# Kernel optimization log

Hardware: AMD Instinct MI355X
Metric: run time of the kernel (lower is better)

Reference implementation:

```python
import jax, jax.numpy as jnp
import numpy as np
import math

B, S, D, H = 2, 2048, 1024, 16
HD = D // H  # head_dim = 64
ROPE_BASE = 100000
EPS = 1e-09


def _linear_init(key, in_f, out_f):
    std = min(1.0, math.sqrt(out_f / in_f)) / math.sqrt(in_f)
    return jax.random.normal(key, (in_f, out_f)) * std


def setup_inputs() -> dict:
    key = jax.random.key(0)
    ks = jax.random.split(key, 7)
    Q = jax.random.normal(ks[0], (B, S, D), dtype=jnp.float32)
    K = jax.random.normal(ks[1], (B, S, D), dtype=jnp.float32)
    V = jax.random.normal(ks[2], (B, S, D), dtype=jnp.float32)
    mask = jnp.tril(jnp.ones((S, S), dtype=bool))  # causal
    Wq = _linear_init(ks[3], D, D)
    Wk = _linear_init(ks[4], D, D)
    Wv = _linear_init(ks[5], D, D)
    Wo = _linear_init(ks[6], D, D)
    return {"Q": Q, "K": K, "V": V, "mask": mask,
            "Wq": Wq, "Wk": Wk, "Wv": Wv, "Wo": Wo}


def _rope_tables(seq_len, d):
    positions = jnp.arange(0, seq_len)
    freqs = ROPE_BASE ** (jnp.arange(0, d, 2) / d)
    gamma = positions[:, None] * (1.0 / freqs)[None, :]  # [t, d/2]
    return jnp.cos(gamma).astype(jnp.bfloat16), jnp.sin(gamma).astype(jnp.bfloat16)


def _apply_rope(x, cos, sin):
    # x: [..., t, d]; cos/sin: [t, d/2]
    d = x.shape[-1]
    x1, x2 = x[..., : d // 2], x[..., d // 2:]
    y1 = x1 * cos + x2 * sin
    y2 = -x1 * sin + x2 * cos
    return jnp.concatenate([y1, y2], axis=-1)


def _rms_norm(x):
    rms = jnp.sqrt(jnp.mean(jnp.square(x), axis=-1, keepdims=True) + EPS)
    return x / rms


def reference(Q, K, V, mask, Wq, Wk, Wv, Wo):
    cos, sin = _rope_tables(S, HD)
    q = jnp.dot(Q, Wq)
    k = jnp.dot(K, Wk)
    v = jnp.dot(V, Wv)
    # [B, S, D] -> [B, H, S, HD]
    split = lambda t: t.reshape(*t.shape[:-1], H, HD).swapaxes(-3, -2)
    q, k, v = split(q), split(k), split(v)
    q = _rms_norm(_apply_rope(q, cos, sin))
    k = _rms_norm(_apply_rope(k, cos, sin))
    logits = jnp.einsum('bhqd,bhkd->bhqk', q, k) / jnp.sqrt(jnp.float32(HD))
    logits = jnp.where(mask[None, None, :, :], logits, -1000000000.0)
    attn = jax.nn.softmax(logits, axis=-1)
    vals = jnp.einsum('bhqk,bhkd->bhqd', attn, v)
    # [B, H, S, HD] -> [B, S, D]
    vals = vals.swapaxes(-3, -2).reshape(B, S, D)
    return jnp.dot(vals, Wo)
```

## Files before the change

### kernel.cpp

```cpp
#include <hip/hip_runtime.h>
#include <hip/hip_bf16.h>
#include <stdint.h>

typedef __hip_bfloat16 bf16;
typedef __attribute__((ext_vector_type(8))) short short8;
typedef __attribute__((ext_vector_type(4))) short short4v;
typedef __attribute__((ext_vector_type(4))) float float4v;

static constexpr int nB = 2, nS = 2048, nD = 1024, nH = 16, nHD = 64;
static constexpr int nBS = nB * nS;

#define AS_GLOBAL __attribute__((address_space(1)))
#define AS_LDS    __attribute__((address_space(3)))

union Frag16B { short8 v; uint4 u4; uint2 u2[2]; };

__device__ __forceinline__ void gload_lds16(const void* g, void* l) {
  __builtin_amdgcn_global_load_lds((AS_GLOBAL uint32_t*)(g), (AS_LDS uint32_t*)(l), 16, 0, 0);
}

__device__ __forceinline__ float fast_exp2(float x) {
#if __has_builtin(__builtin_amdgcn_exp2f)
  return __builtin_amdgcn_exp2f(x);
#else
  float r; asm volatile("v_exp_f32 %0, %1" : "=v"(r) : "v"(x)); return r;
#endif
}

__device__ __forceinline__ void lds_barrier() {
  asm volatile("s_waitcnt lgkmcnt(0)\ns_barrier" ::: "memory");
}

__device__ __forceinline__ void lgkm_wait() {
  asm volatile("s_waitcnt lgkmcnt(0)" ::: "memory");
}

__global__ __launch_bounds__(256) void prep_kernel(
    const float* __restrict__ Qin, const float* __restrict__ Kin, const float* __restrict__ Vin,
    const float* __restrict__ Wq, const float* __restrict__ Wk,
    const float* __restrict__ Wv, const float* __restrict__ Wo,
    bf16* __restrict__ Qbf, bf16* __restrict__ Kbf, bf16* __restrict__ Vbf,
    bf16* __restrict__ WqT, bf16* __restrict__ WkT, bf16* __restrict__ WvT, bf16* __restrict__ WoT,
    bf16* __restrict__ cos_t, bf16* __restrict__ sin_t) {
  __shared__ float tile[64][65];
  int bx = blockIdx.x, t = threadIdx.x;
  if (bx < 3072) {
    int tz = bx >> 10, blk = bx & 1023;
    const float* src = tz == 0 ? Qin : tz == 1 ? Kin : Vin;
    bf16* dst = tz == 0 ? Qbf : tz == 1 ? Kbf : Vbf;
#pragma unroll
    for (int i = 0; i < 4; ++i) {
      int idx = blk * 1024 + i * 256 + t;
      float4 v = ((const float4*)src)[idx];
      union { bf16 b[4]; uint2 u; } tmp;
      tmp.b[0] = __float2bfloat16(v.x);
      tmp.b[1] = __float2bfloat16(v.y);
      tmp.b[2] = __float2bfloat16(v.z);
      tmp.b[3] = __float2bfloat16(v.w);
      ((uint2*)dst)[idx] = tmp.u;
    }
  } else if (bx < 4096) {
    int idx = bx - 3072;
    int z = idx >> 8;
    const float* W = z == 0 ? Wq : z == 1 ? Wk : z == 2 ? Wv : Wo;
    bf16* T = z == 0 ? WqT : z == 1 ? WkT : z == 2 ? WvT : WoT;
    int tk = (idx & 15) * 64, tn = ((idx >> 4) & 15) * 64;
    int c = t & 63, r0 = t >> 6;
#pragma unroll
    for (int i = 0; i < 16; ++i) {
      int r = i * 4 + r0;
      tile[r][c] = W[(size_t)(tk + r) * nD + tn + c];
    }
    __syncthreads();
#pragma unroll
    for (int i = 0; i < 16; ++i) {
      int r = i * 4 + r0;
      T[(size_t)(tn + r) * nD + tk + c] = __float2bfloat16(tile[c][r]);
    }
  } else {
    int base = (bx - 4096) * 1024 + t * 4;
#pragma unroll
    for (int i = 0; i < 4; ++i) {
      int e = base + i;
      int s = e >> 5, j = e & 31;
      float inv_freq = powf(100000.0f, -(float)(2 * j) / 64.0f);
      float g = (float)s * inv_freq;
      cos_t[e] = __float2bfloat16(cosf(g));
      sin_t[e] = __float2bfloat16(sinf(g));
    }
  }
}

__global__ __launch_bounds__(512, 2) void gemm_qkv_kernel(
    const bf16* __restrict__ A0, const bf16* __restrict__ A1, const bf16* __restrict__ A2,
    const bf16* __restrict__ Bt0, const bf16* __restrict__ Bt1, const bf16* __restrict__ Bt2,
    bf16* __restrict__ q_h, bf16* __restrict__ k_h, bf16* __restrict__ vt_h,
    const bf16* __restrict__ cos_t, const bf16* __restrict__ sin_t) {
  const int z = blockIdx.z;
  const bf16* __restrict__ A  = z == 0 ? A0 : (z == 1 ? A1 : A2);
  const bf16* __restrict__ Bt = z == 0 ? Bt0 : (z == 1 ? Bt1 : Bt2);

  __shared__ bf16 As[2 * 256 * 32];
  __shared__ bf16 Bs[2 * 256 * 32];

  const int t = threadIdx.x;
  const int lane = t & 63;
  const int wid = t >> 6;
  const int quad = lane >> 4;
  const int l16 = lane & 15;
  const int wm = wid >> 2;
  const int wn = wid & 3;
  const int m0 = blockIdx.x * 256;
  const int n0 = blockIdx.y * 256;

  const int sc    = (t & 7) ^ ((t >> 3) & 7);
  const int sml   = 2 * (t >> 3) + (sc >> 2);
  const int skoff = (sc & 3) * 8;
  const int swave = wid * 512;

  const int R0a = wm * 64 + (l16 >> 1);
  const int R0b = wn * 32 + (l16 >> 1);
  const int cpar = (l16 & 1) * 4;
  const int abase = R0a * 64 + (((cpar + quad) ^ (R0a & 7)) * 8);
  const int bbase = R0b * 64 + (((cpar + quad) ^ (R0b & 7)) * 8);

#define STAGE_A(KT, BUF) do { \
    const bf16* ag_ = A + (size_t)(m0 + sml) * nD + (KT) * 32 + skoff; \
    gload_lds16(ag_, As + (BUF) + swave); \
    gload_lds16(ag_ + (size_t)128 * nD, As + (BUF) + 4096 + swave); \
  } while (0)
#define STAGE_B(KT, BUF) do { \
    const bf16* bg_ = Bt + (size_t)(n0 + sml) * nD + (KT) * 32 + skoff; \
    gload_lds16(bg_, Bs + (BUF) + swave); \
    gload_lds16(bg_ + (size_t)128 * nD, Bs + (BUF) + 4096 + swave); \
  } while (0)

  float4v acc[8][4] = {};

  STAGE_A(0, 0);
  STAGE_B(0, 0);
  STAGE_A(1, 8192);
  asm volatile("s_waitcnt vmcnt(2)" ::: "memory");
  __builtin_amdgcn_s_barrier();

#pragma unroll 2
  for (int T = 0; T < 32; ++T) {
    const int cu = (T & 1) * 8192;
    const int nx = cu ^ 8192;

    if (T < 31) STAGE_B(T + 1, nx);
    Frag16B fa[4], fb[4];
#pragma unroll
    for (int mi = 0; mi < 4; ++mi) fa[mi].u4 = *(const uint4*)&As[cu + abase + mi * 512];
#pragma unroll
    for (int ni = 0; ni < 4; ++ni) fb[ni].u4 = *(const uint4*)&Bs[cu + bbase + ni * 512];
    __builtin_amdgcn_s_setprio(1);
#pragma unroll
    for (int mi = 0; mi < 4; ++mi)
#pragma unroll
      for (int ni = 0; ni < 4; ++ni)
        acc[mi][ni] = __builtin_amdgcn_mfma_f32_16x16x32_bf16(fa[mi].v, fb[ni].v, acc[mi][ni], 0, 0, 0);
    __builtin_amdgcn_s_setprio(0);
    __builtin_amdgcn_s_barrier();

    Frag16B fa2[4];
#pragma unroll
    for (int mi = 0; mi < 4; ++mi) fa2[mi].u4 = *(const uint4*)&As[cu + abase + (mi + 4) * 512];
    asm volatile("s_waitcnt lgkmcnt(0)" ::: "memory");
    __builtin_amdgcn_s_setprio(1);
#pragma unroll
    for (int mi = 0; mi < 2; ++mi)
#pragma unroll
      for (int ni = 0; ni < 4; ++ni)
        acc[4 + mi][ni] = __builtin_amdgcn_mfma_f32_16x16x32_bf16(fa2[mi].v, fb[ni].v, acc[4 + mi][ni], 0, 0, 0);
    __builtin_amdgcn_s_setprio(0);
    __builtin_amdgcn_s_barrier();

    if (T < 30) STAGE_A(T + 2, cu);
    __builtin_amdgcn_s_setprio(1);
#pragma unroll
    for (int mi = 2; mi < 4; ++mi)
#pragma unroll
      for (int ni = 0; ni < 4; ++ni)
        acc[4 + mi][ni] = __builtin_amdgcn_mfma_f32_16x16x32_bf16(fa2[mi].v, fb[ni].v, acc[4 + mi][ni], 0, 0, 0);
    __builtin_amdgcn_s_setprio(0);
    if (T < 30) { asm volatile("s_waitcnt vmcnt(2)" ::: "memory"); }
    else        { asm volatile("s_waitcnt vmcnt(0)" ::: "memory"); }
    __builtin_amdgcn_s_barrier();
  }
#undef STAGE_A
#undef STAGE_B

  const int col0 = n0 + wn * 64;
  if (z <= 1) {
    bf16* dst = z ? k_h : q_h;
#pragma unroll
    for (int mi = 0; mi < 8; ++mi)
#pragma unroll
      for (int r = 0; r < 4; ++r) {
        int row = m0 + wm * 128 + mi * 16 + quad * 4 + r;
        int s = row & (nS - 1);
        float x0 = acc[mi][0][r], x1 = acc[mi][1][r], x2 = acc[mi][2][r], x3 = acc[mi][3][r];
        float y[4];
#pragma unroll
        for (int p = 0; p < 2; ++p) {
          int d = p * 16 + l16;
          float c = __bfloat162float(cos_t[s * 32 + d]);
          float sn = __bfloat162float(sin_t[s * 32 + d]);
          float xa = p ? x1 : x0, xb = p ? x3 : x2;
          y[p] = xa * c + xb * sn;
          y[p + 2] = xb * c - xa * sn;
        }
        float ss = y[0] * y[0] + y[1] * y[1] + y[2] * y[2] + y[3] * y[3];
#pragma unroll
        for (int m = 1; m <= 8; m <<= 1) ss += __shfl_xor(ss, m, 64);
        float inv = 1.0f / sqrtf(ss * (1.0f / 64.0f) + 1e-9f);
#pragma unroll
        for (int ni = 0; ni < 4; ++ni)
          dst[(size_t)row * nD + col0 + ni * 16 + l16] = __float2bfloat16(y[ni] * inv);
      }
  } else {
#pragma unroll
    for (int mi = 0; mi < 8; ++mi)
#pragma unroll
      for (int r = 0; r < 4; ++r) {
        int row = m0 + wm * 128 + mi * 16 + quad * 4 + r;
        int b = row >> 11, s = row & (nS - 1);
#pragma unroll
        for (int ni = 0; ni < 4; ++ni) {
          int col = col0 + ni * 16 + l16;
          int h = col >> 6, d = col & 63;
          vt_h[((size_t)((b * nH + h) * 64 + d)) * nS + s] = __float2bfloat16(acc[mi][ni][r]);
        }
      }
  }
}

__global__ __launch_bounds__(256) void gemm_out_kernel(
    const bf16* __restrict__ A, const bf16* __restrict__ Bt, float* __restrict__ C) {
  __shared__ bf16 As[64 * 64];
  __shared__ bf16 Bs[128 * 64];
  const int t = threadIdx.x;
  const int lane = t & 63;
  const int wid = t >> 6;
  const int quad = lane >> 4;
  const int l16 = lane & 15;
  const int wm = wid >> 1;
  const int wn = wid & 1;
  const int m0 = blockIdx.x * 64;
  const int n0 = blockIdx.y * 128;
  const int K = nD;
  const int rloc = lane >> 3, cl = lane & 7;
  const int cg = cl ^ rloc;

  float4v acc[2][4] = {};
  for (int kt = 0; kt < K; kt += 64) {
    __syncthreads();
#pragma unroll
    for (int p = 0; p < 2; ++p) {
      int rowbase = (p * 4 + wid) * 8;
      gload_lds16(A + (size_t)(m0 + rowbase + rloc) * K + kt + cg * 8, As + (size_t)rowbase * 64);
    }
#pragma unroll
    for (int p = 0; p < 4; ++p) {
      int rowbase = (p * 4 + wid) * 8;
      gload_lds16(Bt + (size_t)(n0 + rowbase + rloc) * K + kt + cg * 8, Bs + (size_t)rowbase * 64);
    }
    __syncthreads();

#pragma unroll
    for (int ks = 0; ks < 2; ++ks) {
      Frag16B a[2], b[4];
#pragma unroll
      for (int mi = 0; mi < 2; ++mi) {
        int row = wm * 32 + mi * 16 + l16;
        int ch = (ks * 4 + quad) ^ (row & 7);
        a[mi].u4 = *(const uint4*)&As[row * 64 + ch * 8];
      }
#pragma unroll
      for (int ni = 0; ni < 4; ++ni) {
        int row = wn * 64 + ni * 16 + l16;
        int ch = (ks * 4 + quad) ^ (row & 7);
        b[ni].u4 = *(const uint4*)&Bs[row * 64 + ch * 8];
      }
#pragma unroll
      for (int mi = 0; mi < 2; ++mi)
#pragma unroll
        for (int ni = 0; ni < 4; ++ni)
          acc[mi][ni] = __builtin_amdgcn_mfma_f32_16x16x32_bf16(a[mi].v, b[ni].v, acc[mi][ni], 0, 0, 0);
    }
  }
#pragma unroll
  for (int mi = 0; mi < 2; ++mi)
#pragma unroll
    for (int ni = 0; ni < 4; ++ni)
#pragma unroll
      for (int r = 0; r < 4; ++r) {
        int row = m0 + wm * 32 + mi * 16 + quad * 4 + r;
        int col = n0 + wn * 64 + ni * 16 + l16;
        C[(size_t)row * nD + col] = acc[mi][ni][r];
      }
}

static constexpr float SC = 0.18033688011112042f;

__global__ __launch_bounds__(512, 4) void attn_kernel(const bf16* __restrict__ q_h,
                                                      const bf16* __restrict__ k_h,
                                                      const bf16* __restrict__ vt_h,
                                                      bf16* __restrict__ vals) {
  __shared__ bf16 lds_buf[4 * 4096];

  const int t = threadIdx.x;
  const int lane = t & 63, wid = t >> 6, quad = lane >> 4, l16 = lane & 15;
  const int id = blockIdx.x;
  const int xcd = id & 7;
  const int j = id >> 3;
  const int jj = j & 31;
  const int bh = xcd * 4 + (jj & 3);
  const int u = jj >> 2;
  const int qt = (j < 32) ? (15 - u) : u;
  const int b = bh >> 4, h = bh & 15;

  const bf16* Kbase = k_h + ((size_t)b * nS) * nD + h * 64;
  const bf16* Vbase = vt_h + (size_t)bh * 64 * nS;

  const int rl = lane >> 3;
  const int cg8 = ((lane & 7) ^ rl) * 8;
  const int srow = wid * 8 + rl;
  const int r7 = l16 & 7;

  bf16* const scratch = lds_buf + wid * 1152;

  const int nkt = 2 * qt + 2;
  const int q0w = qt * 128 + wid * 16;

  Frag16B qf[2];
  {
    const bf16* qp = q_h + ((size_t)(b * nS + q0w + l16)) * nD + h * 64;
    qf[0].u4 = *(const uint4*)(qp + quad * 8);
    qf[1].u4 = *(const uint4*)(qp + 32 + quad * 8);
  }

#define STAGE_KV(KT) do { \
    const int bo_ = ((KT) & 1) * 4096; \
    gload_lds16(Kbase + (size_t)((KT) * 64 + srow) * nD + cg8, lds_buf + bo_ + wid * 512); \
    gload_lds16(Vbase + (size_t)srow * nS + (KT) * 64 + cg8, lds_buf + 8192 + bo_ + wid * 512); \
  } while (0)

  STAGE_KV(0);
  asm volatile("s_waitcnt vmcnt(0)" ::: "memory");
  __builtin_amdgcn_s_barrier();

  float4v o_acc[4] = {};
  float l_acc = 0.f;

  for (int kt = 0; kt < nkt; ++kt) {
    if (kt + 1 < nkt) STAGE_KV(kt + 1);

    const bf16* Kb = lds_buf + (kt & 1) * 4096;
    const bf16* Vb = lds_buf + 8192 + (kt & 1) * 4096;

    if (kt * 64 <= q0w + 15) {
      float4v st[4];
      __builtin_amdgcn_s_setprio(1);
#pragma unroll
      for (int kt4 = 0; kt4 < 4; ++kt4) {
        int row = kt4 * 16 + l16;
        Frag16B k0, k1;
        k0.u4 = *(const uint4*)&Kb[row * 64 + ((quad ^ r7) * 8)];
        k1.u4 = *(const uint4*)&Kb[row * 64 + (((quad + 4) ^ r7) * 8)];
        float4v zz = {};
        zz = __builtin_amdgcn_mfma_f32_16x16x32_bf16(k0.v, qf[0].v, zz, 0, 0, 0);
        st[kt4] = __builtin_amdgcn_mfma_f32_16x16x32_bf16(k1.v, qf[1].v, zz, 0, 0, 0);
      }
      __builtin_amdgcn_s_setprio(0);

      short4v pf[4];
      const bool need_mask = (kt * 64 + 63) > q0w;
      if (need_mask) {
        int qg = q0w + l16;
#pragma unroll
        for (int kt4 = 0; kt4 < 4; ++kt4) {
          int key0 = kt * 64 + kt4 * 16 + quad * 4;
#pragma unroll
          for (int r = 0; r < 4; ++r) {
            float x = st[kt4][r] * SC;
            if (key0 + r > qg) x = -12000.0f;
            float p = fast_exp2(x);
            l_acc += p;
            union { bf16 hh; short ss; } cv;
            cv.hh = __float2bfloat16(p);
            pf[kt4][r] = cv.ss;
          }
        }
      } else {
#pragma unroll
        for (int kt4 = 0; kt4 < 4; ++kt4)
#pragma unroll
          for (int r = 0; r < 4; ++r) {
            float p = fast_exp2(st[kt4][r] * SC);
            l_acc += p;
            union { bf16 hh; short ss; } cv;
            cv.hh = __float2bfloat16(p);
            pf[kt4][r] = cv.ss;
          }
      }

      __builtin_amdgcn_s_setprio(1);
#pragma unroll
      for (int dt = 0; dt < 4; ++dt) {
        int row = dt * 16 + l16;
#pragma unroll
        for (int kt4 = 0; kt4 < 4; ++kt4) {
          int chunk = kt4 * 2 + (quad >> 1);
          union { uint2 u; short4v s; } vv;
          vv.u = *(const uint2*)&Vb[row * 64 + ((chunk ^ r7) * 8) + (quad & 1) * 4];
          o_acc[dt] = __builtin_amdgcn_mfma_f32_16x16x16bf16_1k(vv.s, pf[kt4], o_acc[dt], 0, 0, 0);
        }
      }
      __builtin_amdgcn_s_setprio(0);
    }

    asm volatile("s_waitcnt vmcnt(0) lgkmcnt(0)" ::: "memory");
    __builtin_amdgcn_s_barrier();
  }
#undef STAGE_KV

  float la = l_acc;
  la += __shfl_xor(la, 16, 64);
  la += __shfl_xor(la, 32, 64);
  float inv_l = 1.0f / la;
#pragma unroll
  for (int dt = 0; dt < 4; ++dt) {
    union { bf16 b2[2]; uint u; } p01, p23;
    p01.b2[0] = __float2bfloat16(o_acc[dt][0] * inv_l);
    p01.b2[1] = __float2bfloat16(o_acc[dt][1] * inv_l);
    p23.b2[0] = __float2bfloat16(o_acc[dt][2] * inv_l);
    p23.b2[1] = __float2bfloat16(o_acc[dt][3] * inv_l);
    *(uint*)&scratch[l16 * 72 + dt * 16 + quad * 4] = p01.u;
    *(uint*)&scratch[l16 * 72 + dt * 16 + quad * 4 + 2] = p23.u;
  }
  lgkm_wait();
  uint4 r0 = *(const uint4*)&scratch[l16 * 72 + quad * 16];
  uint4 r1 = *(const uint4*)&scratch[l16 * 72 + quad * 16 + 8];
  int qrow = q0w + l16;
  bf16* vp = vals + ((size_t)(b * nS + qrow)) * nD + h * 64 + quad * 16;
  *(uint4*)(vp) = r0;
  *(uint4*)(vp + 8) = r1;
}

extern "C" void kernel_launch(void* const* d_in, const int* in_sizes, int n_in,
                              void* d_out, int out_size, void* d_ws, size_t ws_size,
                              hipStream_t stream) {
  const float* Qin = (const float*)d_in[0];
  const float* Kin = (const float*)d_in[1];
  const float* Vin = (const float*)d_in[2];
  const float* Wq = (const float*)d_in[4];
  const float* Wk = (const float*)d_in[5];
  const float* Wv = (const float*)d_in[6];
  const float* Wo = (const float*)d_in[7];
  float* out = (float*)d_out;

  char* ws = (char*)d_ws;
  const size_t MB = 1u << 20;
  bf16* Qbf = (bf16*)(ws + 0 * MB);
  bf16* Kbf = (bf16*)(ws + 8 * MB);
  bf16* Vbf = (bf16*)(ws + 16 * MB);
  bf16* WqT = (bf16*)(ws + 24 * MB);
  bf16* WkT = (bf16*)(ws + 26 * MB);
  bf16* WvT = (bf16*)(ws + 28 * MB);
  bf16* WoT = (bf16*)(ws + 30 * MB);
  bf16* cos_t = (bf16*)(ws + 32 * MB);
  bf16* sin_t = (bf16*)(ws + 33 * MB);
  bf16* q_h = (bf16*)(ws + 34 * MB);
  bf16* k_h = (bf16*)(ws + 42 * MB);
  bf16* vt_h = (bf16*)(ws + 50 * MB);
  bf16* vals = (bf16*)(ws + 58 * MB);

  prep_kernel<<<4160, 256, 0, stream>>>(Qin, Kin, Vin, Wq, Wk, Wv, Wo,
                                        Qbf, Kbf, Vbf, WqT, WkT, WvT, WoT, cos_t, sin_t);

  gemm_qkv_kernel<<<dim3(16, 4, 3), 512, 0, stream>>>(Qbf, Kbf, Vbf, WqT, WkT, WvT,
                                                      q_h, k_h, vt_h, cos_t, sin_t);

  attn_kernel<<<512, 512, 0, stream>>>(q_h, k_h, vt_h, vals);

  gemm_out_kernel<<<dim3(64, 8), 256, 0, stream>>>(vals, WoT, out);
}
```

Before: 223.2 us.

## Process 128-key tiles per iteration and peel causal diagonal tile

Doubles the key/value tile staged per loop iteration from 64 to 128 keys, which halves the number of barrier and wait synchronisations. The fully visible tiles now run without any mask checks, and the diagonal tile is peeled into a separate epilogue where only the upper warps compute the second half. LDS use doubles, which may reduce occupancy under the 512-thread, 4-block launch bounds. A barrier is added before the scratch reuse, since scratch overlaps the staging buffer.

```diff
diff --git a/kernel.cpp b/kernel.cpp
--- a/kernel.cpp
+++ b/kernel.cpp
@@ -308,7 +308,7 @@
                                                       const bf16* __restrict__ k_h,
                                                       const bf16* __restrict__ vt_h,
                                                       bf16* __restrict__ vals) {
-  __shared__ bf16 lds_buf[4 * 4096];
+  __shared__ bf16 lds_buf[4 * 8192];
 
   const int t = threadIdx.x;
   const int lane = t & 63, wid = t >> 6, quad = lane >> 4, l16 = lane & 15;
@@ -326,12 +326,10 @@
 
   const int rl = lane >> 3;
   const int cg8 = ((lane & 7) ^ rl) * 8;
-  const int srow = wid * 8 + rl;
   const int r7 = l16 & 7;
 
   bf16* const scratch = lds_buf + wid * 1152;
 
-  const int nkt = 2 * qt + 2;
   const int q0w = qt * 128 + wid * 16;
 
   Frag16B qf[2];
@@ -342,9 +340,71 @@
   }
 
 #define STAGE_KV(KT) do { \
-    const int bo_ = ((KT) & 1) * 4096; \
-    gload_lds16(Kbase + (size_t)((KT) * 64 + srow) * nD + cg8, lds_buf + bo_ + wid * 512); \
-    gload_lds16(Vbase + (size_t)srow * nS + (KT) * 64 + cg8, lds_buf + 8192 + bo_ + wid * 512); \
+    const int bo_ = ((KT) & 1) * 8192; \
+    const bf16* kg_ = Kbase + (size_t)((KT) * 128 + wid * 16 + rl) * nD + cg8; \
+    gload_lds16(kg_, lds_buf + bo_ + wid * 1024); \
+    gload_lds16(kg_ + (size_t)8 * nD, lds_buf + bo_ + wid * 1024 + 512); \
+    const bf16* vg_ = Vbase + (size_t)(wid * 8 + rl) * nS + (KT) * 128 + cg8; \
+    gload_lds16(vg_, lds_buf + 16384 + bo_ + wid * 512); \
+    gload_lds16(vg_ + 64, lds_buf + 16384 + bo_ + 4096 + wid * 512); \
+  } while (0)
+
+#define QKH(Kb, HB, ST) do { \
+    _Pragma("unroll") \
+    for (int kt4 = 0; kt4 < 4; ++kt4) { \
+      int row = (HB) * 64 + kt4 * 16 + l16; \
+      Frag16B k0_, k1_; \
+      k0_.u4 = *(const uint4*)&(Kb)[row * 64 + ((quad ^ r7) * 8)]; \
+      k1_.u4 = *(const uint4*)&(Kb)[row * 64 + (((quad + 4) ^ r7) * 8)]; \
+      float4v zz_ = {}; \
+      zz_ = __builtin_amdgcn_mfma_f32_16x16x32_bf16(k0_.v, qf[0].v, zz_, 0, 0, 0); \
+      (ST)[kt4] = __builtin_amdgcn_mfma_f32_16x16x32_bf16(k1_.v, qf[1].v, zz_, 0, 0, 0); \
+    } \
+  } while (0)
+
+#define EXPH(ST, PF) do { \
+    _Pragma("unroll") \
+    for (int kt4 = 0; kt4 < 4; ++kt4) \
+      _Pragma("unroll") \
+      for (int r = 0; r < 4; ++r) { \
+        float p_ = fast_exp2((ST)[kt4][r] * SC); \
+        l_acc += p_; \
+        union { bf16 hh; short ss; } cv_; \
+        cv_.hh = __float2bfloat16(p_); \
+        (PF)[kt4][r] = cv_.ss; \
+      } \
+  } while (0)
+
+#define EXPHM(ST, PF, HB) do { \
+    int qg_ = q0w + l16; \
+    _Pragma("unroll") \
+    for (int kt4 = 0; kt4 < 4; ++kt4) { \
+      int key0_ = qt * 128 + (HB) * 64 + kt4 * 16 + quad * 4; \
+      _Pragma("unroll") \
+      for (int r = 0; r < 4; ++r) { \
+        float x_ = (ST)[kt4][r] * SC; \
+        if (key0_ + r > qg_) x_ = -12000.0f; \
+        float p_ = fast_exp2(x_); \
+        l_acc += p_; \
+        union { bf16 hh; short ss; } cv_; \
+        cv_.hh = __float2bfloat16(p_); \
+        (PF)[kt4][r] = cv_.ss; \
+      } \
+    } \
+  } while (0)
+
+#define PVH(Vb, HB, PF) do { \
+    _Pragma("unroll") \
+    for (int dt = 0; dt < 4; ++dt) { \
+      int row = dt * 16 + l16; \
+      _Pragma("unroll") \
+      for (int kt4 = 0; kt4 < 4; ++kt4) { \
+        int chunk_ = kt4 * 2 + (quad >> 1); \
+        union { uint2 u; short4v s; } vv_; \
+        vv_.u = *(const uint2*)&(Vb)[(HB) * 4096 + row * 64 + ((chunk_ ^ r7) * 8) + (quad & 1) * 4]; \
+        o_acc[dt] = __builtin_amdgcn_mfma_f32_16x16x16bf16_1k(vv_.s, (PF)[kt4], o_acc[dt], 0, 0, 0); \
+      } \
+    } \
   } while (0)
 
   STAGE_KV(0);
@@ -354,77 +414,55 @@
   float4v o_acc[4] = {};
   float l_acc = 0.f;
 
-  for (int kt = 0; kt < nkt; ++kt) {
-    if (kt + 1 < nkt) STAGE_KV(kt + 1);
-
-    const bf16* Kb = lds_buf + (kt & 1) * 4096;
-    const bf16* Vb = lds_buf + 8192 + (kt & 1) * 4096;
-
-    if (kt * 64 <= q0w + 15) {
-      float4v st[4];
-      __builtin_amdgcn_s_setprio(1);
-#pragma unroll
-      for (int kt4 = 0; kt4 < 4; ++kt4) {
-        int row = kt4 * 16 + l16;
-        Frag16B k0, k1;
-        k0.u4 = *(const uint4*)&Kb[row * 64 + ((quad ^ r7) * 8)];
-        k1.u4 = *(const uint4*)&Kb[row * 64 + (((quad + 4) ^ r7) * 8)];
-        float4v zz = {};
-        zz = __builtin_amdgcn_mfma_f32_16x16x32_bf16(k0.v, qf[0].v, zz, 0, 0, 0);
-        st[kt4] = __builtin_amdgcn_mfma_f32_16x16x32_bf16(k1.v, qf[1].v, zz, 0, 0, 0);
-      }
-      __builtin_amdgcn_s_setprio(0);
-
-      short4v pf[4];
-      const bool need_mask = (kt * 64 + 63) > q0w;
-      if (need_mask) {
-        int qg = q0w + l16;
-#pragma unroll
-        for (int kt4 = 0; kt4 < 4; ++kt4) {
-          int key0 = kt * 64 + kt4 * 16 + quad * 4;
-#pragma unroll
-          for (int r = 0; r < 4; ++r) {
-            float x = st[kt4][r] * SC;
-            if (key0 + r > qg) x = -12000.0f;
-            float p = fast_exp2(x);
-            l_acc += p;
-            union { bf16 hh; short ss; } cv;
-            cv.hh = __float2bfloat16(p);
-            pf[kt4][r] = cv.ss;
-          }
-        }
-      } else {
-#pragma unroll
-        for (int kt4 = 0; kt4 < 4; ++kt4)
-#pragma unroll
-          for (int r = 0; r < 4; ++r) {
-            float p = fast_exp2(st[kt4][r] * SC);
-            l_acc += p;
-            union { bf16 hh; short ss; } cv;
-            cv.hh = __float2bfloat16(p);
-            pf[kt4][r] = cv.ss;
-          }
-      }
-
-      __builtin_amdgcn_s_setprio(1);
-#pragma unroll
-      for (int dt = 0; dt < 4; ++dt) {
-        int row = dt * 16 + l16;
-#pragma unroll
-        for (int kt4 = 0; kt4 < 4; ++kt4) {
-          int chunk = kt4 * 2 + (quad >> 1);
-          union { uint2 u; short4v s; } vv;
-          vv.u = *(const uint2*)&Vb[row * 64 + ((chunk ^ r7) * 8) + (quad & 1) * 4];
-          o_acc[dt] = __builtin_amdgcn_mfma_f32_16x16x16bf16_1k(vv.s, pf[kt4], o_acc[dt], 0, 0, 0);
-        }
-      }
-      __builtin_amdgcn_s_setprio(0);
-    }
+  for (int kt = 0; kt < qt; ++kt) {
+    STAGE_KV(kt + 1);
+    const bf16* Kb = lds_buf + (kt & 1) * 8192;
+    const bf16* Vb = lds_buf + 16384 + (kt & 1) * 8192;
+
+    float4v st0[4], st1[4];
+    __builtin_amdgcn_s_setprio(1);
+    QKH(Kb, 0, st0);
+    QKH(Kb, 1, st1);
+    __builtin_amdgcn_s_setprio(0);
+
+    short4v pf[4];
+    EXPH(st0, pf);
+    __builtin_amdgcn_s_setprio(1);
+    PVH(Vb, 0, pf);
+    __builtin_amdgcn_s_setprio(0);
+    EXPH(st1, pf);
+    __builtin_amdgcn_s_setprio(1);
+    PVH(Vb, 1, pf);
+    __builtin_amdgcn_s_setprio(0);
 
     asm volatile("s_waitcnt vmcnt(0) lgkmcnt(0)" ::: "memory");
     __builtin_amdgcn_s_barrier();
   }
+
+  {
+    const bf16* Kb = lds_buf + (qt & 1) * 8192;
+    const bf16* Vb = lds_buf + 16384 + (qt & 1) * 8192;
+
+    float4v st0[4];
+    QKH(Kb, 0, st0);
+    short4v pf[4];
+    EXPHM(st0, pf, 0);
+    PVH(Vb, 0, pf);
+
+    if (wid >= 4) {
+      float4v st1[4];
+      QKH(Kb, 1, st1);
+      EXPHM(st1, pf, 1);
+      PVH(Vb, 1, pf);
+    }
+  }
 #undef STAGE_KV
+#undef QKH
+#undef EXPH
+#undef EXPHM
+#undef PVH
+
+  lds_barrier();
 
   float la = l_acc;
   la += __shfl_xor(la, 16, 64);
```

Result: faster. 213.9 us (-4.1%).
